# Kernel tuning notes

Measured on AMD Instinct MI355X. Metric: run time of the kernel, lower is better.

The kernel has to match this reference:

```python
import jax, jax.numpy as jnp
import numpy as np

B, N, DIN, DOUT, H, DH, DC, NL, L = 8, 256, 64, 64, 8, 8, 64, 32, 2
SCALE = DH ** -0.5  # out_dim-per-head scaling used by both attention variants


def _ln(x, g, b):
    m = jnp.mean(x, -1, keepdims=True)
    v = jnp.mean((x - m) ** 2, -1, keepdims=True)
    return (x - m) * jax.lax.rsqrt(v + 1e-5) * g + b


def _cross_attn(x, ctx, mask_b, wq, wkv, wo, bo):
    # CrossAttentionLayer: standard softmax attention with clamp(-5,5)
    b, n, _ = x.shape
    m = ctx.shape[1]
    q = (x @ wq).reshape(b, n, H, DH).transpose(0, 2, 1, 3)
    k, v = jnp.split(ctx @ wkv, 2, axis=-1)
    k = k.reshape(b, m, H, DH).transpose(0, 2, 1, 3)
    v = v.reshape(b, m, H, DH).transpose(0, 2, 1, 3)
    sim = jnp.einsum('bhid,bhjd->bhij', q, k) * SCALE
    if mask_b is not None:
        sim = jnp.where(mask_b[:, None, None, :], sim, -jnp.finfo(sim.dtype).max)
    sim = jnp.clip(sim, -5.0, 5.0)
    attn = jax.nn.softmax(sim, axis=-1)
    out = jnp.einsum('bhij,bhjd->bhid', attn, v)
    out = out.transpose(0, 2, 1, 3).reshape(b, n, H * DH)
    return out @ wo + bo


def _mha_edge(p, e, k_RW, mask, wq, wk, we, wv):
    # GraphiT MultiHeadAttentionLayer with edge features + k_RW attention PE
    Q = (p @ wq).reshape(B, N, H, DH)
    K = (p @ wk).reshape(B, N, H, DH) * SCALE
    V = (p @ wv).reshape(B, N, H, DH).transpose(0, 2, 1, 3)  # [B,H,N,d]
    E = (e @ we).reshape(B, N, N, H, DH)
    scores = jnp.einsum('bihk,bjhk,bijhk->bhij', Q, K, E)
    scores = jnp.exp(scores - jnp.max(scores, axis=(-2, -1), keepdims=True))
    scores = scores * mask[:, None, :, None] * mask[:, None, None, :]
    scores = scores * k_RW
    denom = jnp.clip(jnp.sum(scores, -1, keepdims=True), 1e-6, None)
    out = jnp.einsum('bhij,bhjd->bhid', scores, V) / denom
    return out.transpose(0, 2, 1, 3).reshape(B, N, H * DH)


def setup_inputs() -> dict:
    key = jax.random.key(0)
    ks = jax.random.split(key, 32)
    rn = lambda k, s: jax.random.normal(k, s, dtype=jnp.float32)
    inp = {
        'h': rn(ks[0], (B, N, DIN)),
        'p': rn(ks[1], (B, N, DIN)),
        'e': rn(ks[2], (B, N, N, DIN)),
        'k_RW': jax.random.uniform(ks[3], (B, 1, N, N), dtype=jnp.float32),
        'queries': rn(ks[4], (B, NL, DC)),
        'mask': jnp.ones((B, N), dtype=jnp.float32),
        # attention_p (MultiHeadAttentionLayer) weights
        'wq_p': rn(ks[5], (DIN, H * DH)) * 0.05,
        'wk_p': rn(ks[6], (DIN, H * DH)) * 0.05,
        'we_p': rn(ks[7], (DIN, H * DH)) * 0.05,
        'wv_p': rn(ks[8], (DIN, H * DH)) * 0.05,
        'wo_p': rn(ks[9], (DOUT, DOUT)) * 0.05,
        # cross_attention_h (queries attend to nodes)
        'cq_wq': rn(ks[10], (DC, H * DH)) * 0.05,
        'cq_wkv': rn(ks[11], (DIN, 2 * H * DH)) * 0.05,
        'cq_wo': rn(ks[12], (H * DH, DC)) * 0.05,
        'cq_bo': jnp.zeros((DC,), dtype=jnp.float32),
        # L_cross latent self-attention layers (stacked)
        'sa_wq': rn(ks[13], (L, DC, H * DH)) * 0.05,
        'sa_wkv': rn(ks[14], (L, DC, 2 * H * DH)) * 0.05,
        'sa_wo': rn(ks[15], (L, H * DH, DC)) * 0.05,
        'sa_bo': jnp.zeros((L, DC), dtype=jnp.float32),
        # O_queries, norms, FFN
        'oq_w': rn(ks[16], (DC, DC)) * 0.05,
        'ln1_g': jnp.ones((DC,), dtype=jnp.float32),
        'ln1_b': jnp.zeros((DC,), dtype=jnp.float32),
        'ffn_w1': rn(ks[17], (DC, 2 * DC)) * 0.05,
        'ffn_w2': rn(ks[18], (2 * DC, DC)) * 0.05,
        'ln2_g': jnp.ones((DC,), dtype=jnp.float32),
        'ln2_b': jnp.zeros((DC,), dtype=jnp.float32),
    }
    return inp


def reference(h, p, e, k_RW, queries, mask,
              wq_p, wk_p, we_p, wv_p, wo_p,
              cq_wq, cq_wkv, cq_wo, cq_bo,
              sa_wq, sa_wkv, sa_wo, sa_bo,
              oq_w, ln1_g, ln1_b, ffn_w1, ffn_w2, ln2_g, ln2_b):
    # forward_p: update positional encoding via edge-modulated attention
    p_attn = _mha_edge(p, e, k_RW, mask, wq_p, wk_p, we_p, wv_p)
    p_new = p + jnp.tanh(p_attn @ wo_p)  # residual, no dropout (eval)
    # combine node features with updated PE (use_node_pe='sum')
    h_c = h + p_new
    mask_b = mask > 0.5
    # perceiver cross-attention: latents attend to nodes
    q = queries + _cross_attn(queries, h_c, mask_b, cq_wq, cq_wkv, cq_wo, cq_bo)
    # L_cross latent self-attention blocks with residual
    for i in range(L):
        q = q + _cross_attn(q, q, None, sa_wq[i], sa_wkv[i], sa_wo[i], sa_bo[i])
    # O_queries projection + layer norm
    q = _ln(q @ oq_w, ln1_g, ln1_b)
    # feed-forward block on queries
    ff = jax.nn.relu(q @ ffn_w1) @ ffn_w2
    q = _ln(q + ff, ln2_g, ln2_b)
    return q
```

## Files before the change

kernel.cpp:

```cpp
#include <hip/hip_runtime.h>
#include <hip/hip_bf16.h>
#include <math.h>

typedef __bf16 bf16x8 __attribute__((ext_vector_type(8)));
typedef float floatx4 __attribute__((ext_vector_type(4)));

#define ATT_SCALE 0.35355339059327373f

__device__ __forceinline__ __bf16 f2b(float x) { return (__bf16)x; }

__global__ void k_proj(const float* __restrict__ p, const float* __restrict__ quer,
                       const float* __restrict__ wq, const float* __restrict__ wk,
                       const float* __restrict__ wv, const float* __restrict__ cq_wq,
                       float* __restrict__ Q, float* __restrict__ Ks,
                       float* __restrict__ V, float* __restrict__ q1) {
  int blk = blockIdx.x, t = threadIdx.x;
  __shared__ float xr[64];
  if (blk < 2048) {
    xr[t] = p[blk * 64 + t];
    __syncthreads();
    float aq = 0.f, ak = 0.f, av = 0.f;
    for (int c = 0; c < 64; c++) {
      float x = xr[c];
      aq += x * wq[c * 64 + t];
      ak += x * wk[c * 64 + t];
      av += x * wv[c * 64 + t];
    }
    Q[blk * 64 + t] = aq;
    Ks[blk * 64 + t] = ak * ATT_SCALE;
    V[blk * 64 + t] = av;
  } else {
    int r = blk - 2048;
    xr[t] = quer[r * 64 + t];
    __syncthreads();
    float a = 0.f;
    for (int c = 0; c < 64; c++) a += xr[c] * cq_wq[c * 64 + t];
    q1[r * 64 + t] = a;
  }
}

__global__ __launch_bounds__(256) void k_edge(
    const float* __restrict__ e, const float* __restrict__ we,
    const float* __restrict__ krw, const float* __restrict__ mask,
    const float* __restrict__ hin, const float* __restrict__ pin,
    const float* __restrict__ wo, const float* __restrict__ cq_wkv,
    const float* __restrict__ Q, const float* __restrict__ Ks,
    const float* __restrict__ V, float* __restrict__ Kc, float* __restrict__ Vc) {
  int bi = blockIdx.x;
  int b = bi >> 8;
  int t = threadIdx.x;
  int w = t >> 6, l = t & 63;
  int l15 = l & 15, quad = l >> 4, half8 = (l >> 3) & 1, d = l & 7;

  bf16x8 wfrag[4][2];
  for (int nt = 0; nt < 4; nt++)
    for (int kc = 0; kc < 2; kc++)
      for (int jj = 0; jj < 8; jj++)
        wfrag[nt][kc][jj] = f2b(we[(kc * 32 + quad * 8 + jj) * 64 + nt * 16 + l15]);

  float qv[4];
  for (int nt = 0; nt < 4; nt++) qv[nt] = Q[bi * 64 + nt * 16 + l15];
  float mi = mask[bi];

  float aout[4] = {0.f, 0.f, 0.f, 0.f};
  float aden[4] = {0.f, 0.f, 0.f, 0.f};

  for (int mt = 0; mt < 4; mt++) {
    int j0 = w * 64 + mt * 16;
    const float* ep = e + ((long)bi * 256 + j0 + l15) * 64 + quad * 8;
    float4 ea = *reinterpret_cast<const float4*>(ep);
    float4 eb4 = *reinterpret_cast<const float4*>(ep + 4);
    float4 ec = *reinterpret_cast<const float4*>(ep + 32);
    float4 ed4 = *reinterpret_cast<const float4*>(ep + 36);
    bf16x8 a0, a1;
    a0[0] = f2b(ea.x); a0[1] = f2b(ea.y); a0[2] = f2b(ea.z); a0[3] = f2b(ea.w);
    a0[4] = f2b(eb4.x); a0[5] = f2b(eb4.y); a0[6] = f2b(eb4.z); a0[7] = f2b(eb4.w);
    a1[0] = f2b(ec.x); a1[1] = f2b(ec.y); a1[2] = f2b(ec.z); a1[3] = f2b(ec.w);
    a1[4] = f2b(ed4.x); a1[5] = f2b(ed4.y); a1[6] = f2b(ed4.z); a1[7] = f2b(ed4.w);

    int jr0 = j0 + quad * 4;
    float krw_r[4], mj_r[4];
    for (int r = 0; r < 4; r++) {
      krw_r[r] = krw[(long)bi * 256 + jr0 + r];
      mj_r[r] = mask[b * 256 + jr0 + r];
    }
    for (int nt = 0; nt < 4; nt++) {
      floatx4 acc = {0.f, 0.f, 0.f, 0.f};
      acc = __builtin_amdgcn_mfma_f32_16x16x32_bf16(a0, wfrag[nt][0], acc, 0, 0, 0);
      acc = __builtin_amdgcn_mfma_f32_16x16x32_bf16(a1, wfrag[nt][1], acc, 0, 0, 0);
      int hk = nt * 16 + l15;
      int hbase = hk & 56;
      for (int r = 0; r < 4; r++) {
        int jr = jr0 + r;
        float s = acc[r] * qv[nt] * Ks[(b * 256 + jr) * 64 + hk];
        s += __shfl_xor(s, 1);
        s += __shfl_xor(s, 2);
        s += __shfl_xor(s, 4);
        float wg = __expf(s) * krw_r[r] * mj_r[r];
        aden[nt] += wg;
        aout[nt] += wg * V[(b * 256 + jr) * 64 + hbase + d];
      }
    }
  }
  for (int nt = 0; nt < 4; nt++) {
    float o = aout[nt], dn = aden[nt];
    o += __shfl_xor(o, 16); o += __shfl_xor(o, 32);
    dn += __shfl_xor(dn, 16); dn += __shfl_xor(dn, 32);
    aout[nt] = o; aden[nt] = dn;
  }

  __shared__ float red[4][64];
  __shared__ float redden[4][8];
  __shared__ float pav[64];
  __shared__ float hcl[64];
  if (l < 16) {
    for (int nt = 0; nt < 4; nt++) {
      int head = nt * 2 + half8;
      red[w][head * 8 + d] = aout[nt];
      if (d == 0) redden[w][head] = aden[nt];
    }
  }
  __syncthreads();
  if (t < 64) {
    int head = t >> 3;
    float num = red[0][t] + red[1][t] + red[2][t] + red[3][t];
    float den = redden[0][head] + redden[1][head] + redden[2][head] + redden[3][head];
    num *= mi;
    den = fmaxf(den * mi, 1e-6f);
    pav[t] = num / den;
  }
  __syncthreads();
  if (t < 64) {
    float a = 0.f;
    for (int c = 0; c < 64; c++) a += pav[c] * wo[c * 64 + t];
    hcl[t] = hin[bi * 64 + t] + pin[bi * 64 + t] + tanhf(a);
  }
  __syncthreads();
  if (t < 128) {
    float a = 0.f;
    for (int c = 0; c < 64; c++) a += hcl[c] * cq_wkv[c * 128 + t];
    if (t < 64) Kc[bi * 64 + t] = a;
    else        Vc[bi * 64 + t - 64] = a;
  }
}

__global__ void k_cross(const float* __restrict__ q1, const float* __restrict__ Kc,
                        const float* __restrict__ Vc, const float* __restrict__ mask,
                        float* __restrict__ oc) {
  int bh = blockIdx.x, b = bh >> 3, h = bh & 7;
  int t = threadIdx.x, r = t >> 3, g = t & 7;
  __shared__ float qL[32][8];
  qL[r][g] = q1[(b * 32 + r) * 64 + h * 8 + g];
  __syncthreads();
  float num[8] = {0.f, 0.f, 0.f, 0.f, 0.f, 0.f, 0.f, 0.f};
  float den = 0.f;
  for (int jj = 0; jj < 32; jj++) {
    int j = jj * 8 + g;
    const float* kp = Kc + (b * 256 + j) * 64 + h * 8;
    float s = 0.f;
    for (int dd = 0; dd < 8; dd++) s += qL[r][dd] * kp[dd];
    s *= ATT_SCALE;
    float mj = mask[b * 256 + j];
    s = (mj > 0.5f) ? s : -1e30f;
    s = fminf(fmaxf(s, -5.f), 5.f);
    float ex = __expf(s);
    den += ex;
    const float* vp = Vc + (b * 256 + j) * 64 + h * 8;
    for (int dd = 0; dd < 8; dd++) num[dd] += ex * vp[dd];
  }
  den += __shfl_xor(den, 1); den += __shfl_xor(den, 2); den += __shfl_xor(den, 4);
  for (int dd = 0; dd < 8; dd++) {
    float v = num[dd];
    v += __shfl_xor(v, 1); v += __shfl_xor(v, 2); v += __shfl_xor(v, 4);
    num[dd] = v;
  }
  oc[(b * 32 + r) * 64 + h * 8 + g] = num[g] / den;
}

__global__ void k_projqkv(const float* __restrict__ attn_in, const float* __restrict__ Wo,
                          const float* __restrict__ bo, const float* __restrict__ residp,
                          const float* __restrict__ wql, const float* __restrict__ wkvl,
                          float* __restrict__ q_out, float* __restrict__ qq,
                          float* __restrict__ kvb) {
  int r = blockIdx.x, t = threadIdx.x;
  __shared__ float oL[64];
  __shared__ float qL[64];
  oL[t] = attn_in[r * 64 + t];
  __syncthreads();
  float a = 0.f;
  for (int c = 0; c < 64; c++) a += oL[c] * Wo[c * 64 + t];
  float qvv = residp[r * 64 + t] + a + bo[t];
  q_out[r * 64 + t] = qvv;
  qL[t] = qvv;
  __syncthreads();
  float aq = 0.f, ak = 0.f, av = 0.f;
  for (int c = 0; c < 64; c++) {
    float x = qL[c];
    aq += x * wql[c * 64 + t];
    ak += x * wkvl[c * 128 + t];
    av += x * wkvl[c * 128 + 64 + t];
  }
  qq[r * 64 + t] = aq;
  kvb[r * 128 + t] = ak;
  kvb[r * 128 + 64 + t] = av;
}

__global__ void k_sattn(const float* __restrict__ qq, const float* __restrict__ kvb,
                        float* __restrict__ os) {
  int bh = blockIdx.x, b = bh >> 3, h = bh & 7;
  int t = threadIdx.x, r = t >> 3, g = t & 7;
  __shared__ float qL[32][8];
  qL[r][g] = qq[(b * 32 + r) * 64 + h * 8 + g];
  __syncthreads();
  float num[8] = {0.f, 0.f, 0.f, 0.f, 0.f, 0.f, 0.f, 0.f};
  float den = 0.f;
  for (int jj = 0; jj < 4; jj++) {
    int j = jj * 8 + g;
    const float* kp = kvb + (b * 32 + j) * 128 + h * 8;
    float s = 0.f;
    for (int dd = 0; dd < 8; dd++) s += qL[r][dd] * kp[dd];
    s *= ATT_SCALE;
    s = fminf(fmaxf(s, -5.f), 5.f);
    float ex = __expf(s);
    den += ex;
    for (int dd = 0; dd < 8; dd++) num[dd] += ex * kp[64 + dd];
  }
  den += __shfl_xor(den, 1); den += __shfl_xor(den, 2); den += __shfl_xor(den, 4);
  for (int dd = 0; dd < 8; dd++) {
    float v = num[dd];
    v += __shfl_xor(v, 1); v += __shfl_xor(v, 2); v += __shfl_xor(v, 4);
    num[dd] = v;
  }
  os[(b * 32 + r) * 64 + h * 8 + g] = num[g] / den;
}

__global__ void k_final(const float* __restrict__ os, const float* __restrict__ Wo,
                        const float* __restrict__ bo, const float* __restrict__ qprev,
                        const float* __restrict__ oqw, const float* __restrict__ g1,
                        const float* __restrict__ b1, const float* __restrict__ w1,
                        const float* __restrict__ w2, const float* __restrict__ g2,
                        const float* __restrict__ b2v, float* __restrict__ out) {
  int r = blockIdx.x, t = threadIdx.x;
  __shared__ float oL[64];
  __shared__ float q2L[64];
  __shared__ float yL[64];
  __shared__ float hhs[128];
  oL[t] = os[r * 64 + t];
  __syncthreads();
  float a = 0.f;
  for (int c = 0; c < 64; c++) a += oL[c] * Wo[c * 64 + t];
  float q2 = qprev[r * 64 + t] + a + bo[t];
  q2L[t] = q2;
  __syncthreads();
  float x = 0.f;
  for (int c = 0; c < 64; c++) x += q2L[c] * oqw[c * 64 + t];
  float m = x;
  for (int off = 1; off < 64; off <<= 1) m += __shfl_xor(m, off);
  m *= (1.f / 64.f);
  float dv = x - m, vv = dv * dv;
  for (int off = 1; off < 64; off <<= 1) vv += __shfl_xor(vv, off);
  vv *= (1.f / 64.f);
  float y = dv * rsqrtf(vv + 1e-5f) * g1[t] + b1[t];
  yL[t] = y;
  __syncthreads();
  float h1 = 0.f, h2 = 0.f;
  for (int c = 0; c < 64; c++) {
    float xx = yL[c];
    h1 += xx * w1[c * 128 + t];
    h2 += xx * w1[c * 128 + 64 + t];
  }
  hhs[t] = fmaxf(h1, 0.f);
  hhs[t + 64] = fmaxf(h2, 0.f);
  __syncthreads();
  float ff = 0.f;
  for (int c = 0; c < 128; c++) ff += hhs[c] * w2[c * 64 + t];
  float z = y + ff;
  float m2 = z;
  for (int off = 1; off < 64; off <<= 1) m2 += __shfl_xor(m2, off);
  m2 *= (1.f / 64.f);
  float dz = z - m2, v2 = dz * dz;
  for (int off = 1; off < 64; off <<= 1) v2 += __shfl_xor(v2, off);
  v2 *= (1.f / 64.f);
  float z2 = dz * rsqrtf(v2 + 1e-5f) * g2[t] + b2v[t];
  out[r * 64 + t] = z2;
}

extern "C" void kernel_launch(void* const* d_in, const int* in_sizes, int n_in,
                              void* d_out, int out_size, void* d_ws, size_t ws_size,
                              hipStream_t stream) {
  const float* h_in   = (const float*)d_in[0];
  const float* p_in   = (const float*)d_in[1];
  const float* e_in   = (const float*)d_in[2];
  const float* krw    = (const float*)d_in[3];
  const float* quer   = (const float*)d_in[4];
  const float* mask   = (const float*)d_in[5];
  const float* wq_p   = (const float*)d_in[6];
  const float* wk_p   = (const float*)d_in[7];
  const float* we_p   = (const float*)d_in[8];
  const float* wv_p   = (const float*)d_in[9];
  const float* wo_p   = (const float*)d_in[10];
  const float* cq_wq  = (const float*)d_in[11];
  const float* cq_wkv = (const float*)d_in[12];
  const float* cq_wo  = (const float*)d_in[13];
  const float* cq_bo  = (const float*)d_in[14];
  const float* sa_wq  = (const float*)d_in[15];
  const float* sa_wkv = (const float*)d_in[16];
  const float* sa_wo  = (const float*)d_in[17];
  const float* sa_bo  = (const float*)d_in[18];
  const float* oq_w   = (const float*)d_in[19];
  const float* ln1_g  = (const float*)d_in[20];
  const float* ln1_b  = (const float*)d_in[21];
  const float* ffn_w1 = (const float*)d_in[22];
  const float* ffn_w2 = (const float*)d_in[23];
  const float* ln2_g  = (const float*)d_in[24];
  const float* ln2_b  = (const float*)d_in[25];

  float* ws = (float*)d_ws;
  float* Q   = ws;
  float* Ks  = Q + 131072;
  float* V   = Ks + 131072;
  float* q1  = V + 131072;
  float* Kc  = q1 + 16384;
  float* Vc  = Kc + 131072;
  float* oc  = Vc + 131072;
  float* q0  = oc + 16384;
  float* qq  = q0 + 16384;
  float* kvb = qq + 16384;
  float* osa = kvb + 32768;
  float* qc1 = osa + 16384;

  k_proj<<<2304, 64, 0, stream>>>(p_in, quer, wq_p, wk_p, wv_p, cq_wq, Q, Ks, V, q1);
  k_edge<<<2048, 256, 0, stream>>>(e_in, we_p, krw, mask, h_in, p_in, wo_p, cq_wkv,
                                   Q, Ks, V, Kc, Vc);
  k_cross<<<64, 256, 0, stream>>>(q1, Kc, Vc, mask, oc);
  k_projqkv<<<256, 64, 0, stream>>>(oc, cq_wo, cq_bo, quer,
                                    sa_wq, sa_wkv, q0, qq, kvb);
  k_sattn<<<64, 256, 0, stream>>>(qq, kvb, osa);
  k_projqkv<<<256, 64, 0, stream>>>(osa, sa_wo, sa_bo, q0,
                                    sa_wq + 4096, sa_wkv + 8192, qc1, qq, kvb);
  k_sattn<<<64, 256, 0, stream>>>(qq, kvb, osa);
  k_final<<<256, 64, 0, stream>>>(osa, sa_wo + 4096, sa_bo + 64, qc1, oq_w,
                                  ln1_g, ln1_b, ffn_w1, ffn_w2, ln2_g, ln2_b,
                                  (float*)d_out);
}
```

Before: 311.2 us.

## Fuse perceiver tail into one kernel and transpose edge MFMA operand mapping

```diff
diff --git a/kernel.cpp b/kernel.cpp
--- a/kernel.cpp
+++ b/kernel.cpp
@@ -8,6 +8,15 @@
 #define ATT_SCALE 0.35355339059327373f
 
 __device__ __forceinline__ __bf16 f2b(float x) { return (__bf16)x; }
+
+#define FMA8(A, X, WP) do {                                    \
+    const float4 _wa = *(const float4*)(WP);                   \
+    const float4 _wb = *(const float4*)((WP) + 4);             \
+    A[0] += (X) * _wa.x; A[1] += (X) * _wa.y;                  \
+    A[2] += (X) * _wa.z; A[3] += (X) * _wa.w;                  \
+    A[4] += (X) * _wb.x; A[5] += (X) * _wb.y;                  \
+    A[6] += (X) * _wb.z; A[7] += (X) * _wb.w;                  \
+  } while (0)
 
 __global__ void k_proj(const float* __restrict__ p, const float* __restrict__ quer,
                        const float* __restrict__ wq, const float* __restrict__ wk,
@@ -50,7 +59,8 @@
   int b = bi >> 8;
   int t = threadIdx.x;
   int w = t >> 6, l = t & 63;
-  int l15 = l & 15, quad = l >> 4, half8 = (l >> 3) & 1, d = l & 7;
+  int l15 = l & 15, quad = l >> 4;
+  int hsel = quad >> 1;
 
   bf16x8 wfrag[4][2];
   for (int nt = 0; nt < 4; nt++)
@@ -58,16 +68,24 @@
       for (int jj = 0; jj < 8; jj++)
         wfrag[nt][kc][jj] = f2b(we[(kc * 32 + quad * 8 + jj) * 64 + nt * 16 + l15]);
 
-  float qv[4];
-  for (int nt = 0; nt < 4; nt++) qv[nt] = Q[bi * 64 + nt * 16 + l15];
+  float4 qv[4];
+#pragma unroll
+  for (int nt = 0; nt < 4; nt++)
+    qv[nt] = *(const float4*)(Q + bi * 64 + nt * 16 + quad * 4);
+
   float mi = mask[bi];
 
-  float aout[4] = {0.f, 0.f, 0.f, 0.f};
+  float aout[4][8];
   float aden[4] = {0.f, 0.f, 0.f, 0.f};
-
-  for (int mt = 0; mt < 4; mt++) {
-    int j0 = w * 64 + mt * 16;
-    const float* ep = e + ((long)bi * 256 + j0 + l15) * 64 + quad * 8;
+#pragma unroll
+  for (int nt = 0; nt < 4; nt++)
+#pragma unroll
+    for (int d = 0; d < 8; d++) aout[nt][d] = 0.f;
+
+  for (int jt = 0; jt < 4; jt++) {
+    int j0 = w * 64 + jt * 16;
+    int j = j0 + l15;
+    const float* ep = e + ((long)bi * 256 + j) * 64 + quad * 8;
     float4 ea = *reinterpret_cast<const float4*>(ep);
     float4 eb4 = *reinterpret_cast<const float4*>(ep + 4);
     float4 ec = *reinterpret_cast<const float4*>(ep + 32);
@@ -78,46 +96,56 @@
     a1[0] = f2b(ec.x); a1[1] = f2b(ec.y); a1[2] = f2b(ec.z); a1[3] = f2b(ec.w);
     a1[4] = f2b(ed4.x); a1[5] = f2b(ed4.y); a1[6] = f2b(ed4.z); a1[7] = f2b(ed4.w);
 
-    int jr0 = j0 + quad * 4;
-    float krw_r[4], mj_r[4];
-    for (int r = 0; r < 4; r++) {
-      krw_r[r] = krw[(long)bi * 256 + jr0 + r];
-      mj_r[r] = mask[b * 256 + jr0 + r];
-    }
+    float kwm = krw[(long)bi * 256 + j] * mask[b * 256 + j];
+    const float* ksrow = Ks + ((long)(b * 256 + j)) * 64 + quad * 4;
+    const float* vrow0 = V + ((long)(b * 256 + j)) * 64 + hsel * 8;
+
+#pragma unroll
     for (int nt = 0; nt < 4; nt++) {
       floatx4 acc = {0.f, 0.f, 0.f, 0.f};
-      acc = __builtin_amdgcn_mfma_f32_16x16x32_bf16(a0, wfrag[nt][0], acc, 0, 0, 0);
-      acc = __builtin_amdgcn_mfma_f32_16x16x32_bf16(a1, wfrag[nt][1], acc, 0, 0, 0);
-      int hk = nt * 16 + l15;
-      int hbase = hk & 56;
-      for (int r = 0; r < 4; r++) {
-        int jr = jr0 + r;
-        float s = acc[r] * qv[nt] * Ks[(b * 256 + jr) * 64 + hk];
-        s += __shfl_xor(s, 1);
-        s += __shfl_xor(s, 2);
-        s += __shfl_xor(s, 4);
-        float wg = __expf(s) * krw_r[r] * mj_r[r];
-        aden[nt] += wg;
-        aout[nt] += wg * V[(b * 256 + jr) * 64 + hbase + d];
-      }
-    }
-  }
+      acc = __builtin_amdgcn_mfma_f32_16x16x32_bf16(wfrag[nt][0], a0, acc, 0, 0, 0);
+      acc = __builtin_amdgcn_mfma_f32_16x16x32_bf16(wfrag[nt][1], a1, acc, 0, 0, 0);
+      float4 kf = *(const float4*)(ksrow + nt * 16);
+      float s = acc[0] * kf.x * qv[nt].x + acc[1] * kf.y * qv[nt].y +
+                acc[2] * kf.z * qv[nt].z + acc[3] * kf.w * qv[nt].w;
+      s += __shfl_xor(s, 16);
+      float wg = __expf(s) * kwm;
+      aden[nt] += wg;
+      const float4 va = *(const float4*)(vrow0 + nt * 16);
+      const float4 vb = *(const float4*)(vrow0 + nt * 16 + 4);
+      aout[nt][0] += wg * va.x; aout[nt][1] += wg * va.y;
+      aout[nt][2] += wg * va.z; aout[nt][3] += wg * va.w;
+      aout[nt][4] += wg * vb.x; aout[nt][5] += wg * vb.y;
+      aout[nt][6] += wg * vb.z; aout[nt][7] += wg * vb.w;
+    }
+  }
+
+#pragma unroll
   for (int nt = 0; nt < 4; nt++) {
-    float o = aout[nt], dn = aden[nt];
-    o += __shfl_xor(o, 16); o += __shfl_xor(o, 32);
-    dn += __shfl_xor(dn, 16); dn += __shfl_xor(dn, 32);
-    aout[nt] = o; aden[nt] = dn;
+    float dn = aden[nt];
+    dn += __shfl_xor(dn, 1); dn += __shfl_xor(dn, 2);
+    dn += __shfl_xor(dn, 4); dn += __shfl_xor(dn, 8);
+    aden[nt] = dn;
+#pragma unroll
+    for (int d = 0; d < 8; d++) {
+      float o = aout[nt][d];
+      o += __shfl_xor(o, 1); o += __shfl_xor(o, 2);
+      o += __shfl_xor(o, 4); o += __shfl_xor(o, 8);
+      aout[nt][d] = o;
+    }
   }
 
   __shared__ float red[4][64];
   __shared__ float redden[4][8];
   __shared__ float pav[64];
   __shared__ float hcl[64];
-  if (l < 16) {
+  if (l15 == 0 && (quad & 1) == 0) {
+#pragma unroll
     for (int nt = 0; nt < 4; nt++) {
-      int head = nt * 2 + half8;
-      red[w][head * 8 + d] = aout[nt];
-      if (d == 0) redden[w][head] = aden[nt];
+      int head = nt * 2 + hsel;
+#pragma unroll
+      for (int d = 0; d < 8; d++) red[w][head * 8 + d] = aout[nt][d];
+      redden[w][head] = aden[nt];
     }
   }
   __syncthreads();
@@ -144,145 +172,252 @@
   }
 }
 
-__global__ void k_cross(const float* __restrict__ q1, const float* __restrict__ Kc,
-                        const float* __restrict__ Vc, const float* __restrict__ mask,
-                        float* __restrict__ oc) {
-  int bh = blockIdx.x, b = bh >> 3, h = bh & 7;
-  int t = threadIdx.x, r = t >> 3, g = t & 7;
-  __shared__ float qL[32][8];
-  qL[r][g] = q1[(b * 32 + r) * 64 + h * 8 + g];
-  __syncthreads();
-  float num[8] = {0.f, 0.f, 0.f, 0.f, 0.f, 0.f, 0.f, 0.f};
-  float den = 0.f;
-  for (int jj = 0; jj < 32; jj++) {
-    int j = jj * 8 + g;
-    const float* kp = Kc + (b * 256 + j) * 64 + h * 8;
-    float s = 0.f;
-    for (int dd = 0; dd < 8; dd++) s += qL[r][dd] * kp[dd];
-    s *= ATT_SCALE;
-    float mj = mask[b * 256 + j];
-    s = (mj > 0.5f) ? s : -1e30f;
-    s = fminf(fmaxf(s, -5.f), 5.f);
-    float ex = __expf(s);
-    den += ex;
-    const float* vp = Vc + (b * 256 + j) * 64 + h * 8;
-    for (int dd = 0; dd < 8; dd++) num[dd] += ex * vp[dd];
-  }
-  den += __shfl_xor(den, 1); den += __shfl_xor(den, 2); den += __shfl_xor(den, 4);
-  for (int dd = 0; dd < 8; dd++) {
-    float v = num[dd];
-    v += __shfl_xor(v, 1); v += __shfl_xor(v, 2); v += __shfl_xor(v, 4);
-    num[dd] = v;
-  }
-  oc[(b * 32 + r) * 64 + h * 8 + g] = num[g] / den;
-}
-
-__global__ void k_projqkv(const float* __restrict__ attn_in, const float* __restrict__ Wo,
-                          const float* __restrict__ bo, const float* __restrict__ residp,
-                          const float* __restrict__ wql, const float* __restrict__ wkvl,
-                          float* __restrict__ q_out, float* __restrict__ qq,
-                          float* __restrict__ kvb) {
-  int r = blockIdx.x, t = threadIdx.x;
-  __shared__ float oL[64];
-  __shared__ float qL[64];
-  oL[t] = attn_in[r * 64 + t];
-  __syncthreads();
-  float a = 0.f;
-  for (int c = 0; c < 64; c++) a += oL[c] * Wo[c * 64 + t];
-  float qvv = residp[r * 64 + t] + a + bo[t];
-  q_out[r * 64 + t] = qvv;
-  qL[t] = qvv;
-  __syncthreads();
-  float aq = 0.f, ak = 0.f, av = 0.f;
-  for (int c = 0; c < 64; c++) {
-    float x = qL[c];
-    aq += x * wql[c * 64 + t];
-    ak += x * wkvl[c * 128 + t];
-    av += x * wkvl[c * 128 + 64 + t];
-  }
-  qq[r * 64 + t] = aq;
-  kvb[r * 128 + t] = ak;
-  kvb[r * 128 + 64 + t] = av;
-}
-
-__global__ void k_sattn(const float* __restrict__ qq, const float* __restrict__ kvb,
-                        float* __restrict__ os) {
-  int bh = blockIdx.x, b = bh >> 3, h = bh & 7;
-  int t = threadIdx.x, r = t >> 3, g = t & 7;
-  __shared__ float qL[32][8];
-  qL[r][g] = qq[(b * 32 + r) * 64 + h * 8 + g];
-  __syncthreads();
-  float num[8] = {0.f, 0.f, 0.f, 0.f, 0.f, 0.f, 0.f, 0.f};
-  float den = 0.f;
-  for (int jj = 0; jj < 4; jj++) {
-    int j = jj * 8 + g;
-    const float* kp = kvb + (b * 32 + j) * 128 + h * 8;
-    float s = 0.f;
-    for (int dd = 0; dd < 8; dd++) s += qL[r][dd] * kp[dd];
-    s *= ATT_SCALE;
-    s = fminf(fmaxf(s, -5.f), 5.f);
-    float ex = __expf(s);
-    den += ex;
-    for (int dd = 0; dd < 8; dd++) num[dd] += ex * kp[64 + dd];
-  }
-  den += __shfl_xor(den, 1); den += __shfl_xor(den, 2); den += __shfl_xor(den, 4);
-  for (int dd = 0; dd < 8; dd++) {
-    float v = num[dd];
-    v += __shfl_xor(v, 1); v += __shfl_xor(v, 2); v += __shfl_xor(v, 4);
-    num[dd] = v;
-  }
-  os[(b * 32 + r) * 64 + h * 8 + g] = num[g] / den;
-}
-
-__global__ void k_final(const float* __restrict__ os, const float* __restrict__ Wo,
-                        const float* __restrict__ bo, const float* __restrict__ qprev,
-                        const float* __restrict__ oqw, const float* __restrict__ g1,
-                        const float* __restrict__ b1, const float* __restrict__ w1,
-                        const float* __restrict__ w2, const float* __restrict__ g2,
-                        const float* __restrict__ b2v, float* __restrict__ out) {
-  int r = blockIdx.x, t = threadIdx.x;
-  __shared__ float oL[64];
-  __shared__ float q2L[64];
-  __shared__ float yL[64];
-  __shared__ float hhs[128];
-  oL[t] = os[r * 64 + t];
-  __syncthreads();
-  float a = 0.f;
-  for (int c = 0; c < 64; c++) a += oL[c] * Wo[c * 64 + t];
-  float q2 = qprev[r * 64 + t] + a + bo[t];
-  q2L[t] = q2;
-  __syncthreads();
-  float x = 0.f;
-  for (int c = 0; c < 64; c++) x += q2L[c] * oqw[c * 64 + t];
-  float m = x;
-  for (int off = 1; off < 64; off <<= 1) m += __shfl_xor(m, off);
-  m *= (1.f / 64.f);
-  float dv = x - m, vv = dv * dv;
-  for (int off = 1; off < 64; off <<= 1) vv += __shfl_xor(vv, off);
-  vv *= (1.f / 64.f);
-  float y = dv * rsqrtf(vv + 1e-5f) * g1[t] + b1[t];
-  yL[t] = y;
-  __syncthreads();
-  float h1 = 0.f, h2 = 0.f;
-  for (int c = 0; c < 64; c++) {
-    float xx = yL[c];
-    h1 += xx * w1[c * 128 + t];
-    h2 += xx * w1[c * 128 + 64 + t];
-  }
-  hhs[t] = fmaxf(h1, 0.f);
-  hhs[t + 64] = fmaxf(h2, 0.f);
-  __syncthreads();
-  float ff = 0.f;
-  for (int c = 0; c < 128; c++) ff += hhs[c] * w2[c * 64 + t];
-  float z = y + ff;
-  float m2 = z;
-  for (int off = 1; off < 64; off <<= 1) m2 += __shfl_xor(m2, off);
-  m2 *= (1.f / 64.f);
-  float dz = z - m2, v2 = dz * dz;
-  for (int off = 1; off < 64; off <<= 1) v2 += __shfl_xor(v2, off);
-  v2 *= (1.f / 64.f);
-  float z2 = dz * rsqrtf(v2 + 1e-5f) * g2[t] + b2v[t];
-  out[r * 64 + t] = z2;
+__global__ __launch_bounds__(256) void k_tail(
+    const float* __restrict__ q1, const float* __restrict__ Kc,
+    const float* __restrict__ Vc, const float* __restrict__ mask,
+    const float* __restrict__ quer,
+    const float* __restrict__ cq_wo, const float* __restrict__ cq_bo,
+    const float* __restrict__ sa_wq, const float* __restrict__ sa_wkv,
+    const float* __restrict__ sa_wo, const float* __restrict__ sa_bo,
+    const float* __restrict__ oq_w, const float* __restrict__ ln1g,
+    const float* __restrict__ ln1b, const float* __restrict__ w1,
+    const float* __restrict__ w2, const float* __restrict__ ln2g,
+    const float* __restrict__ ln2b, float* __restrict__ out) {
+  int b = blockIdx.x, t = threadIdx.x;
+  __shared__ float KT[32][64];
+  __shared__ float VT[32][64];
+  __shared__ float msk[256];
+  __shared__ float ocs[32][64];
+  __shared__ float q0s[32][64];
+  __shared__ float qqs[32][64];
+  __shared__ float qc1s[32][64];
+
+  msk[t] = mask[b * 256 + t];
+
+  int h = t >> 5, r = t & 31;
+  int r2 = t >> 3, c0 = (t & 7) * 8;
+
+  {
+    const float* qp = q1 + (b * 32 + r) * 64 + h * 8;
+    float4 qa = *(const float4*)qp;
+    float4 qb = *(const float4*)(qp + 4);
+    float num[8] = {0.f, 0.f, 0.f, 0.f, 0.f, 0.f, 0.f, 0.f};
+    float den = 0.f;
+    for (int jt = 0; jt < 8; jt++) {
+      __syncthreads();
+      const float* ksrc = Kc + (b * 256 + jt * 32) * 64 + t * 8;
+      const float* vsrc = Vc + (b * 256 + jt * 32) * 64 + t * 8;
+      float4 k0 = *(const float4*)ksrc, k1 = *(const float4*)(ksrc + 4);
+      float4 v0 = *(const float4*)vsrc, v1 = *(const float4*)(vsrc + 4);
+      int rr = t >> 3, cc = (t & 7) * 8;
+      *(float4*)&KT[rr][cc] = k0; *(float4*)&KT[rr][cc + 4] = k1;
+      *(float4*)&VT[rr][cc] = v0; *(float4*)&VT[rr][cc + 4] = v1;
+      __syncthreads();
+      for (int jj = 0; jj < 32; jj++) {
+        float4 ka = *(const float4*)&KT[jj][h * 8];
+        float4 kb = *(const float4*)&KT[jj][h * 8 + 4];
+        float s = qa.x * ka.x + qa.y * ka.y + qa.z * ka.z + qa.w * ka.w +
+                  qb.x * kb.x + qb.y * kb.y + qb.z * kb.z + qb.w * kb.w;
+        s *= ATT_SCALE;
+        float mj = msk[jt * 32 + jj];
+        s = (mj > 0.5f) ? s : -1e30f;
+        s = fminf(fmaxf(s, -5.f), 5.f);
+        float ex = __expf(s);
+        den += ex;
+        float4 va = *(const float4*)&VT[jj][h * 8];
+        float4 vb = *(const float4*)&VT[jj][h * 8 + 4];
+        num[0] += ex * va.x; num[1] += ex * va.y;
+        num[2] += ex * va.z; num[3] += ex * va.w;
+        num[4] += ex * vb.x; num[5] += ex * vb.y;
+        num[6] += ex * vb.z; num[7] += ex * vb.w;
+      }
+    }
+    float inv = 1.f / den;
+#pragma unroll
+    for (int d = 0; d < 8; d++) ocs[r][h * 8 + d] = num[d] * inv;
+  }
+  __syncthreads();
+
+  {
+    float acc[8];
+    const float* rp = quer + (b * 32 + r2) * 64 + c0;
+#pragma unroll
+    for (int o = 0; o < 8; o++) acc[o] = rp[o] + cq_bo[c0 + o];
+    const float* xr = &ocs[r2][0];
+    for (int c = 0; c < 64; c++) FMA8(acc, xr[c], cq_wo + c * 64 + c0);
+#pragma unroll
+    for (int o = 0; o < 8; o++) q0s[r2][c0 + o] = acc[o];
+  }
+  __syncthreads();
+
+  {
+    float aq[8] = {0.f, 0.f, 0.f, 0.f, 0.f, 0.f, 0.f, 0.f};
+    float ak[8] = {0.f, 0.f, 0.f, 0.f, 0.f, 0.f, 0.f, 0.f};
+    float av[8] = {0.f, 0.f, 0.f, 0.f, 0.f, 0.f, 0.f, 0.f};
+    const float* xr = &q0s[r2][0];
+    for (int c = 0; c < 64; c++) {
+      float x = xr[c];
+      FMA8(aq, x, sa_wq + c * 64 + c0);
+      FMA8(ak, x, sa_wkv + c * 128 + c0);
+      FMA8(av, x, sa_wkv + c * 128 + 64 + c0);
+    }
+#pragma unroll
+    for (int o = 0; o < 8; o++) {
+      qqs[r2][c0 + o] = aq[o];
+      KT[r2][c0 + o] = ak[o];
+      VT[r2][c0 + o] = av[o];
+    }
+  }
+  __syncthreads();
+
+#define SATTN(QSRC)                                                          \
+  {                                                                          \
+    const float* qpp = &QSRC[r][h * 8];                                      \
+    float4 sqa = *(const float4*)qpp;                                        \
+    float4 sqb = *(const float4*)(qpp + 4);                                  \
+    float nm[8] = {0.f, 0.f, 0.f, 0.f, 0.f, 0.f, 0.f, 0.f};                  \
+    float dn = 0.f;                                                          \
+    for (int j = 0; j < 32; j++) {                                           \
+      float4 ka = *(const float4*)&KT[j][h * 8];                             \
+      float4 kb = *(const float4*)&KT[j][h * 8 + 4];                         \
+      float s = sqa.x * ka.x + sqa.y * ka.y + sqa.z * ka.z + sqa.w * ka.w +  \
+                sqb.x * kb.x + sqb.y * kb.y + sqb.z * kb.z + sqb.w * kb.w;   \
+      s *= ATT_SCALE;                                                        \
+      s = fminf(fmaxf(s, -5.f), 5.f);                                        \
+      float ex = __expf(s);                                                  \
+      dn += ex;                                                              \
+      float4 va = *(const float4*)&VT[j][h * 8];                             \
+      float4 vb = *(const float4*)&VT[j][h * 8 + 4];                         \
+      nm[0] += ex * va.x; nm[1] += ex * va.y;                                \
+      nm[2] += ex * va.z; nm[3] += ex * va.w;                                \
+      nm[4] += ex * vb.x; nm[5] += ex * vb.y;                                \
+      nm[6] += ex * vb.z; nm[7] += ex * vb.w;                                \
+    }                                                                        \
+    float inv = 1.f / dn;                                                    \
+    _Pragma("unroll")                                                        \
+    for (int d = 0; d < 8; d++) ocs[r][h * 8 + d] = nm[d] * inv;             \
+  }
+
+  SATTN(qqs);
+  __syncthreads();
+
+  {
+    float acc[8];
+#pragma unroll
+    for (int o = 0; o < 8; o++) acc[o] = q0s[r2][c0 + o] + sa_bo[c0 + o];
+    const float* xr = &ocs[r2][0];
+    for (int c = 0; c < 64; c++) FMA8(acc, xr[c], sa_wo + c * 64 + c0);
+#pragma unroll
+    for (int o = 0; o < 8; o++) qc1s[r2][c0 + o] = acc[o];
+  }
+  __syncthreads();
+
+  {
+    float aq[8] = {0.f, 0.f, 0.f, 0.f, 0.f, 0.f, 0.f, 0.f};
+    float ak[8] = {0.f, 0.f, 0.f, 0.f, 0.f, 0.f, 0.f, 0.f};
+    float av[8] = {0.f, 0.f, 0.f, 0.f, 0.f, 0.f, 0.f, 0.f};
+    const float* xr = &qc1s[r2][0];
+    const float* wqL = sa_wq + 4096;
+    const float* wkvL = sa_wkv + 8192;
+    for (int c = 0; c < 64; c++) {
+      float x = xr[c];
+      FMA8(aq, x, wqL + c * 64 + c0);
+      FMA8(ak, x, wkvL + c * 128 + c0);
+      FMA8(av, x, wkvL + c * 128 + 64 + c0);
+    }
+#pragma unroll
+    for (int o = 0; o < 8; o++) {
+      qqs[r2][c0 + o] = aq[o];
+      KT[r2][c0 + o] = ak[o];
+      VT[r2][c0 + o] = av[o];
+    }
+  }
+  __syncthreads();
+
+  SATTN(qqs);
+  __syncthreads();
+
+  {
+    float acc[8];
+#pragma unroll
+    for (int o = 0; o < 8; o++) acc[o] = qc1s[r2][c0 + o] + sa_bo[64 + c0 + o];
+    const float* xr = &ocs[r2][0];
+    const float* woL = sa_wo + 4096;
+    for (int c = 0; c < 64; c++) FMA8(acc, xr[c], woL + c * 64 + c0);
+#pragma unroll
+    for (int o = 0; o < 8; o++) qqs[r2][c0 + o] = acc[o];
+  }
+  __syncthreads();
+
+  float yv[8];
+  {
+    float acc[8] = {0.f, 0.f, 0.f, 0.f, 0.f, 0.f, 0.f, 0.f};
+    const float* xr = &qqs[r2][0];
+    for (int c = 0; c < 64; c++) FMA8(acc, xr[c], oq_w + c * 64 + c0);
+    float sm = acc[0] + acc[1] + acc[2] + acc[3] + acc[4] + acc[5] + acc[6] + acc[7];
+    sm += __shfl_xor(sm, 1); sm += __shfl_xor(sm, 2); sm += __shfl_xor(sm, 4);
+    float mean = sm * 0.015625f;
+    float vs = 0.f;
+#pragma unroll
+    for (int o = 0; o < 8; o++) { float d = acc[o] - mean; vs += d * d; }
+    vs += __shfl_xor(vs, 1); vs += __shfl_xor(vs, 2); vs += __shfl_xor(vs, 4);
+    float rstd = rsqrtf(vs * 0.015625f + 1e-5f);
+#pragma unroll
+    for (int o = 0; o < 8; o++) {
+      yv[o] = (acc[o] - mean) * rstd * ln1g[c0 + o] + ln1b[c0 + o];
+      q0s[r2][c0 + o] = yv[o];
+    }
+  }
+  __syncthreads();
+
+  {
+    int c1 = (t & 7) * 16;
+    float ah[16];
+#pragma unroll
+    for (int o = 0; o < 16; o++) ah[o] = 0.f;
+    const float* xr = &q0s[r2][0];
+    for (int c = 0; c < 64; c++) {
+      float x = xr[c];
+      const float* wp = &w1[c * 128 + c1];
+      float4 wa = *(const float4*)wp;
+      float4 wb = *(const float4*)(wp + 4);
+      float4 wc = *(const float4*)(wp + 8);
+      float4 wd = *(const float4*)(wp + 12);
+      ah[0] += x * wa.x;  ah[1] += x * wa.y;  ah[2] += x * wa.z;  ah[3] += x * wa.w;
+      ah[4] += x * wb.x;  ah[5] += x * wb.y;  ah[6] += x * wb.z;  ah[7] += x * wb.w;
+      ah[8] += x * wc.x;  ah[9] += x * wc.y;  ah[10] += x * wc.z; ah[11] += x * wc.w;
+      ah[12] += x * wd.x; ah[13] += x * wd.y; ah[14] += x * wd.z; ah[15] += x * wd.w;
+    }
+    if (c1 < 64) {
+#pragma unroll
+      for (int o = 0; o < 16; o++) KT[r2][c1 + o] = fmaxf(ah[o], 0.f);
+    } else {
+#pragma unroll
+      for (int o = 0; o < 16; o++) VT[r2][c1 - 64 + o] = fmaxf(ah[o], 0.f);
+    }
+  }
+  __syncthreads();
+
+  {
+    float ff[8] = {0.f, 0.f, 0.f, 0.f, 0.f, 0.f, 0.f, 0.f};
+    for (int c = 0; c < 64; c++) FMA8(ff, KT[r2][c], w2 + c * 64 + c0);
+    for (int c = 0; c < 64; c++) FMA8(ff, VT[r2][c], w2 + (c + 64) * 64 + c0);
+    float z[8];
+#pragma unroll
+    for (int o = 0; o < 8; o++) z[o] = yv[o] + ff[o];
+    float sm = z[0] + z[1] + z[2] + z[3] + z[4] + z[5] + z[6] + z[7];
+    sm += __shfl_xor(sm, 1); sm += __shfl_xor(sm, 2); sm += __shfl_xor(sm, 4);
+    float mean = sm * 0.015625f;
+    float vs = 0.f;
+#pragma unroll
+    for (int o = 0; o < 8; o++) { float d = z[o] - mean; vs += d * d; }
+    vs += __shfl_xor(vs, 1); vs += __shfl_xor(vs, 2); vs += __shfl_xor(vs, 4);
+    float rstd = rsqrtf(vs * 0.015625f + 1e-5f);
+    float* op = out + (b * 32 + r2) * 64 + c0;
+#pragma unroll
+    for (int o = 0; o < 8; o++)
+      op[o] = (z[o] - mean) * rstd * ln2g[c0 + o] + ln2b[c0 + o];
+  }
 }
 
 extern "C" void kernel_launch(void* const* d_in, const int* in_sizes, int n_in,
@@ -322,24 +457,12 @@
   float* q1  = V + 131072;
   float* Kc  = q1 + 16384;
   float* Vc  = Kc + 131072;
-  float* oc  = Vc + 131072;
-  float* q0  = oc + 16384;
-  float* qq  = q0 + 16384;
-  float* kvb = qq + 16384;
-  float* osa = kvb + 32768;
-  float* qc1 = osa + 16384;
 
   k_proj<<<2304, 64, 0, stream>>>(p_in, quer, wq_p, wk_p, wv_p, cq_wq, Q, Ks, V, q1);
   k_edge<<<2048, 256, 0, stream>>>(e_in, we_p, krw, mask, h_in, p_in, wo_p, cq_wkv,
                                    Q, Ks, V, Kc, Vc);
-  k_cross<<<64, 256, 0, stream>>>(q1, Kc, Vc, mask, oc);
-  k_projqkv<<<256, 64, 0, stream>>>(oc, cq_wo, cq_bo, quer,
-                                    sa_wq, sa_wkv, q0, qq, kvb);
-  k_sattn<<<64, 256, 0, stream>>>(qq, kvb, osa);
-  k_projqkv<<<256, 64, 0, stream>>>(osa, sa_wo, sa_bo, q0,
-                                    sa_wq + 4096, sa_wkv + 8192, qc1, qq, kvb);
-  k_sattn<<<64, 256, 0, stream>>>(qq, kvb, osa);
-  k_final<<<256, 64, 0, stream>>>(osa, sa_wo + 4096, sa_bo + 64, qc1, oq_w,
-                                  ln1_g, ln1_b, ffn_w1, ffn_w2, ln2_g, ln2_b,
-                                  (float*)d_out);
+  k_tail<<<8, 256, 0, stream>>>(q1, Kc, Vc, mask, quer, cq_wo, cq_bo,
+                                sa_wq, sa_wkv, sa_wo, sa_bo, oq_w,
+                                ln1_g, ln1_b, ffn_w1, ffn_w2, ln2_g, ln2_b,
+                                (float*)d_out);
 }
```

Result: slower. 480.2 us (+54.3%).
